# Kernel tuning notes

Measured on AMD Instinct MI355X. Metric: run time of the kernel, lower is better.

Reference implementation:

```python
import jax, jax.numpy as jnp
import numpy as np

N, E, D, A, G, S, NG = 100000, 1600000, 64, 64, 64, 4, 16


def setup_inputs() -> dict:
    key = jax.random.key(0)
    ks = jax.random.split(key, 16)
    x = jax.random.normal(ks[0], (N, D), dtype=jnp.float32)
    x_global = jax.random.normal(ks[1], (NG, G), dtype=jnp.float32)
    edge_attr = jax.random.normal(ks[2], (E, 2), dtype=jnp.float32)
    edge_index = jax.random.randint(ks[3], (2, E), 0, N, dtype=jnp.int32)
    batch_ind = jnp.sort(jax.random.randint(ks[4], (N,), 0, NG, dtype=jnp.int32))
    s = lambda fan: 1.0 / np.sqrt(fan)
    Wm = jax.random.normal(ks[5], (S, D, A), dtype=jnp.float32) * s(D)
    bm = jnp.zeros((S, A), dtype=jnp.float32)
    Wa = jax.random.normal(ks[6], (S, D + G + A, D), dtype=jnp.float32) * s(D + G + A)
    ba = jnp.zeros((S, D), dtype=jnp.float32)
    Wgate = jax.random.normal(ks[7], (S, D, 1), dtype=jnp.float32) * s(D)
    bgate = jnp.zeros((S, 1), dtype=jnp.float32)
    Wfeat = jax.random.normal(ks[8], (S, D, D), dtype=jnp.float32) * s(D)
    bfeat = jnp.zeros((S, D), dtype=jnp.float32)
    Wt = jax.random.normal(ks[9], (S, 2 * G, G), dtype=jnp.float32) * s(2 * G)
    bt = jnp.zeros((S, G), dtype=jnp.float32)
    return {
        'x': x, 'x_global': x_global, 'edge_attr': edge_attr,
        'edge_index': edge_index, 'batch_ind': batch_ind, 'num_graphs': NG,
        'Wm': Wm, 'bm': bm, 'Wa': Wa, 'ba': ba,
        'Wgate': Wgate, 'bgate': bgate, 'Wfeat': Wfeat, 'bfeat': bfeat,
        'Wt': Wt, 'bt': bt,
    }


def reference(x, x_global, edge_attr, edge_index, batch_ind, num_graphs,
              Wm, bm, Wa, ba, Wgate, bgate, Wfeat, bfeat, Wt, bt):
    lrelu = jax.nn.leaky_relu  # negative_slope=0.01, matching torch LeakyReLU
    src, dst = edge_index[0], edge_index[1]
    n_nodes = x.shape[0]
    steps = Wm.shape[0]
    for i in range(steps):
        # --- GraphNet step: gather -> edge MLP -> scatter-max ---
        msg = lrelu(x[src] @ Wm[i] + bm[i])                          # [E, A]
        agg = jax.ops.segment_max(msg, dst, num_segments=n_nodes)    # [N, A]
        agg = jnp.where(jnp.isfinite(agg), agg, 0.0)                 # empty segs -> 0
        xg_b = x_global[batch_ind]                                   # [N, G]
        z = jnp.concatenate([x, xg_b, agg], axis=1)                  # [N, D+G+A]
        x = lrelu(z @ Wa[i] + ba[i]) + x                             # residual
        # --- GlobalNode: attentional (segment-softmax) pooling ---
        gate = x @ Wgate[i] + bgate[i]                               # [N, 1]
        gmax = jax.ops.segment_max(gate, batch_ind, num_segments=num_graphs)
        e = jnp.exp(gate - gmax[batch_ind])
        denom = jax.ops.segment_sum(e, batch_ind, num_segments=num_graphs)
        alpha = e / denom[batch_ind]                                 # [N, 1]
        feat = lrelu(x @ Wfeat[i] + bfeat[i])                        # [N, D]
        xg = jax.ops.segment_sum(alpha * feat, batch_ind, num_segments=num_graphs)
        cat = jnp.concatenate([xg, x_global], axis=1)                # [NG, 2G]
        x_global = lrelu(cat @ Wt[i] + bt[i]) + x_global             # residual
    return x, x_global
```

## Files before the change

kernel.cpp:

```cpp
#include <hip/hip_runtime.h>

#define FD 64
#define NSLOPE 0.01f
#define SCAN_BS 1024

__device__ __forceinline__ float lrelu(float v) { return v > 0.f ? v : NSLOPE * v; }

__device__ __forceinline__ unsigned enc_f32(float f) {
    unsigned u = __float_as_uint(f);
    return (u & 0x80000000u) ? ~u : (u | 0x80000000u);
}
__device__ __forceinline__ float dec_f32(unsigned u) {
    return (u & 0x80000000u) ? __uint_as_float(u & 0x7FFFFFFFu) : __uint_as_float(~u);
}


__global__ void k_hist(const int* __restrict__ dst, int* __restrict__ deg, int E)
{
    int e = blockIdx.x * blockDim.x + threadIdx.x;
    if (e < E) atomicAdd(&deg[dst[e]], 1);
}

__global__ void k_scan1(const int* __restrict__ deg, int* __restrict__ off,
                        int* __restrict__ bsums, int N)
{
    __shared__ int tmp[SCAN_BS];
    int t = threadIdx.x, b = blockIdx.x;
    int i = b * SCAN_BS + t;
    int v = (i < N) ? deg[i] : 0;
    tmp[t] = v;
    __syncthreads();
    for (int d = 1; d < SCAN_BS; d <<= 1) {
        int add = (t >= d) ? tmp[t - d] : 0;
        __syncthreads();
        tmp[t] += add;
        __syncthreads();
    }
    if (i < N) off[i] = tmp[t] - v;
    if (t == SCAN_BS - 1) bsums[b] = tmp[t];
}

__global__ void k_scan2(int* __restrict__ bsums, int nb)
{
    __shared__ int tmp[SCAN_BS];
    int t = threadIdx.x;
    int v = (t < nb) ? bsums[t] : 0;
    tmp[t] = v;
    __syncthreads();
    for (int d = 1; d < SCAN_BS; d <<= 1) {
        int add = (t >= d) ? tmp[t - d] : 0;
        __syncthreads();
        tmp[t] += add;
        __syncthreads();
    }
    if (t < nb) bsums[t] = tmp[t] - v;
}

__global__ void k_scan3(int* __restrict__ off, const int* __restrict__ bsums,
                        int* __restrict__ cursor, int N)
{
    int i = blockIdx.x * blockDim.x + threadIdx.x;
    if (i < N) {
        int o = off[i] + bsums[i >> 10];
        off[i] = o;
        cursor[i] = o;
    }
}

__global__ void k_place(const int* __restrict__ src, const int* __restrict__ dst,
                        int* __restrict__ cursor, int* __restrict__ esrc, int E)
{
    int e = blockIdx.x * blockDim.x + threadIdx.x;
    if (e >= E) return;
    int pos = atomicAdd(&cursor[dst[e]], 1);
    esrc[pos] = src[e];
}


__global__ void k_proj(const float* __restrict__ x, const float* __restrict__ Wm,
                       const float* __restrict__ bm, float* __restrict__ p, int N)
{
    int n = blockIdx.x * blockDim.x + threadIdx.x;
    if (n >= N) return;
    const float* xr = x + (size_t)n * FD;
    float acc[FD];
#pragma unroll
    for (int j = 0; j < FD; ++j) acc[j] = bm[j];
    for (int kt = 0; kt < FD / 8; ++kt) {
        float4 a = *(const float4*)(xr + kt * 8);
        float4 b = *(const float4*)(xr + kt * 8 + 4);
        float z8[8] = {a.x, a.y, a.z, a.w, b.x, b.y, b.z, b.w};
#pragma unroll
        for (int kk = 0; kk < 8; ++kk) {
            const float* wrow = Wm + (kt * 8 + kk) * FD;
#pragma unroll
            for (int j = 0; j < FD; ++j) acc[j] += z8[kk] * wrow[j];
        }
    }
    float* pr = p + (size_t)n * FD;
#pragma unroll
    for (int j = 0; j < FD; ++j) pr[j] = acc[j];
}

__global__ void k_agg(const float4* __restrict__ p4, const int* __restrict__ off,
                      const int* __restrict__ endp, const int* __restrict__ esrc,
                      float4* __restrict__ agg4, int N)
{
    int tid = threadIdx.x;
    int q = tid & 15;
    int n = blockIdx.x * 16 + (tid >> 4);
    if (n >= N) return;
    int j0 = off[n], j1 = endp[n];
    float4 m = make_float4(-__builtin_inff(), -__builtin_inff(),
                           -__builtin_inff(), -__builtin_inff());
    int j = j0;
    for (; j + 1 < j1; j += 2) {
        int s0 = esrc[j], s1 = esrc[j + 1];
        float4 v0 = p4[(size_t)s0 * 16 + q];
        float4 v1 = p4[(size_t)s1 * 16 + q];
        m.x = fmaxf(m.x, v0.x); m.y = fmaxf(m.y, v0.y);
        m.z = fmaxf(m.z, v0.z); m.w = fmaxf(m.w, v0.w);
        m.x = fmaxf(m.x, v1.x); m.y = fmaxf(m.y, v1.y);
        m.z = fmaxf(m.z, v1.z); m.w = fmaxf(m.w, v1.w);
    }
    if (j < j1) {
        int s0 = esrc[j];
        float4 v0 = p4[(size_t)s0 * 16 + q];
        m.x = fmaxf(m.x, v0.x); m.y = fmaxf(m.y, v0.y);
        m.z = fmaxf(m.z, v0.z); m.w = fmaxf(m.w, v0.w);
    }
    float4 o;
    if (j0 == j1) o = make_float4(0.f, 0.f, 0.f, 0.f);
    else { o.x = lrelu(m.x); o.y = lrelu(m.y); o.z = lrelu(m.z); o.w = lrelu(m.w); }
    agg4[(size_t)n * 16 + q] = o;
}

__global__ void k_node(const float* __restrict__ x_in, float* __restrict__ x_out,
                       const float* __restrict__ xg, const int* __restrict__ batch,
                       const float* __restrict__ agg,
                       const float* __restrict__ Wa, const float* __restrict__ ba,
                       const float* __restrict__ Wgate, const float* __restrict__ bgate,
                       const float* __restrict__ Wfeat, const float* __restrict__ bfeat,
                       float* __restrict__ gate_out, float* __restrict__ feat_out,
                       unsigned* __restrict__ gmax_enc, int N)
{
    __shared__ unsigned lmax[16];
    int tid = threadIdx.x;
    if (tid < 16) lmax[tid] = 0u;
    __syncthreads();
    int n = blockIdx.x * blockDim.x + tid;
    if (n < N) {
        int g = batch[n];
        const float* xr  = x_in + (size_t)n * FD;
        const float* xgr = xg + (size_t)g * FD;
        const float* ar  = agg + (size_t)n * FD;
        float acc[FD];
#pragma unroll
        for (int j = 0; j < FD; ++j) acc[j] = ba[j];
        for (int kt = 0; kt < 8; ++kt) {
            float4 a = *(const float4*)(xr + kt * 8);
            float4 b = *(const float4*)(xr + kt * 8 + 4);
            float z8[8] = {a.x, a.y, a.z, a.w, b.x, b.y, b.z, b.w};
#pragma unroll
            for (int kk = 0; kk < 8; ++kk) {
                const float* wrow = Wa + (kt * 8 + kk) * FD;
#pragma unroll
                for (int j = 0; j < FD; ++j) acc[j] += z8[kk] * wrow[j];
            }
        }
        for (int kt = 0; kt < 8; ++kt) {
            float4 a = *(const float4*)(xgr + kt * 8);
            float4 b = *(const float4*)(xgr + kt * 8 + 4);
            float z8[8] = {a.x, a.y, a.z, a.w, b.x, b.y, b.z, b.w};
#pragma unroll
            for (int kk = 0; kk < 8; ++kk) {
                const float* wrow = Wa + (64 + kt * 8 + kk) * FD;
#pragma unroll
                for (int j = 0; j < FD; ++j) acc[j] += z8[kk] * wrow[j];
            }
        }
        for (int kt = 0; kt < 8; ++kt) {
            float4 a = *(const float4*)(ar + kt * 8);
            float4 b = *(const float4*)(ar + kt * 8 + 4);
            float z8[8] = {a.x, a.y, a.z, a.w, b.x, b.y, b.z, b.w};
#pragma unroll
            for (int kk = 0; kk < 8; ++kk) {
                const float* wrow = Wa + (128 + kt * 8 + kk) * FD;
#pragma unroll
                for (int j = 0; j < FD; ++j) acc[j] += z8[kk] * wrow[j];
            }
        }
        float gv = bgate[0];
        float* xo = x_out + (size_t)n * FD;
#pragma unroll
        for (int j = 0; j < FD; ++j) {
            float v = lrelu(acc[j]) + xr[j];
            xo[j] = v;
            gv += v * Wgate[j];
        }
        gate_out[n] = gv;
        atomicMax(&lmax[g], enc_f32(gv));
        float acc2[FD];
#pragma unroll
        for (int j = 0; j < FD; ++j) acc2[j] = bfeat[j];
        for (int kt = 0; kt < 8; ++kt) {
            float4 a = *(const float4*)(xo + kt * 8);
            float4 b = *(const float4*)(xo + kt * 8 + 4);
            float z8[8] = {a.x, a.y, a.z, a.w, b.x, b.y, b.z, b.w};
#pragma unroll
            for (int kk = 0; kk < 8; ++kk) {
                const float* wrow = Wfeat + (kt * 8 + kk) * FD;
#pragma unroll
                for (int j = 0; j < FD; ++j) acc2[j] += z8[kk] * wrow[j];
            }
        }
        float* fo = feat_out + (size_t)n * FD;
#pragma unroll
        for (int j = 0; j < FD; ++j) fo[j] = lrelu(acc2[j]);
    }
    __syncthreads();
    if (tid < 16 && lmax[tid] != 0u) atomicMax(&gmax_enc[tid], lmax[tid]);
}

__global__ void k_pool(const float* __restrict__ gate, const float* __restrict__ feat,
                       const int* __restrict__ batch, const unsigned* __restrict__ gmax_enc,
                       float* __restrict__ sum_e, float* __restrict__ Vv, int N)
{
    int gid = blockIdx.x * blockDim.x + threadIdx.x;
    int wave = gid >> 6;
    int lane = threadIdx.x & 63;
    int nwaves = (gridDim.x * blockDim.x) >> 6;
    int chunk = (N + nwaves - 1) / nwaves;
    int n0 = wave * chunk;
    int n1 = min(N, n0 + chunk);
    if (n0 >= n1) return;
    int gcur = batch[n0];
    float gm = dec_f32(gmax_enc[gcur]);
    float accv = 0.f, acce = 0.f;
    for (int n = n0; n < n1; ++n) {
        int g = batch[n];
        if (g != gcur) {
            atomicAdd(&Vv[gcur * FD + lane], accv);
            if (lane == 0) atomicAdd(&sum_e[gcur], acce);
            gcur = g;
            gm = dec_f32(gmax_enc[g]);
            accv = 0.f; acce = 0.f;
        }
        float e = __expf(gate[n] - gm);
        accv += e * feat[(size_t)n * FD + lane];
        acce += e;
    }
    atomicAdd(&Vv[gcur * FD + lane], accv);
    if (lane == 0) atomicAdd(&sum_e[gcur], acce);
}

__global__ void k_global(const float* __restrict__ xg_in, float* __restrict__ xg_out,
                         const float* __restrict__ Vv, const float* __restrict__ sum_e,
                         const float* __restrict__ Wt, const float* __restrict__ bt, int NG)
{
    __shared__ float xgold[1024], xgn[1024];
    int tid = threadIdx.x;
    int tot = NG * FD;
    if (tid < tot) {
        xgold[tid] = xg_in[tid];
        xgn[tid] = Vv[tid] / sum_e[tid >> 6];
    }
    __syncthreads();
    if (tid >= tot) return;
    int g = tid >> 6, j = tid & 63;
    float acc = bt[j];
    for (int k = 0; k < FD; ++k) acc += xgn[g * FD + k] * Wt[k * FD + j];
    for (int k = 0; k < FD; ++k) acc += xgold[g * FD + k] * Wt[(FD + k) * FD + j];
    xg_out[tid] = lrelu(acc) + xgold[tid];
}

extern "C" void kernel_launch(void* const* d_in, const int* in_sizes, int n_in,
                              void* d_out, int out_size, void* d_ws, size_t ws_size,
                              hipStream_t stream)
{
    const float* x0     = (const float*)d_in[0];
    const float* xg0    = (const float*)d_in[1];
    const int*   ei     = (const int*)d_in[3];
    const int*   batch  = (const int*)d_in[4];
    const float* Wm     = (const float*)d_in[6];
    const float* bm     = (const float*)d_in[7];
    const float* Wa     = (const float*)d_in[8];
    const float* ba     = (const float*)d_in[9];
    const float* Wgate  = (const float*)d_in[10];
    const float* bgate  = (const float*)d_in[11];
    const float* Wfeat  = (const float*)d_in[12];
    const float* bfeat  = (const float*)d_in[13];
    const float* Wt     = (const float*)d_in[14];
    const float* bt     = (const float*)d_in[15];

    const int N  = in_sizes[0] / FD;
    const int E  = in_sizes[3] / 2;
    const int NG = in_sizes[1] / FD;
    const int S  = in_sizes[6] / (FD * FD);

    const int* esrc_in = ei;
    const int* edst_in = ei + E;

    float* x_out  = (float*)d_out;
    float* xg_out = (float*)d_out + (size_t)N * FD;

    char* ws = (char*)d_ws;
    const size_t rowB = (size_t)N * FD * 4;
    float* agg   = (float*)ws;
    float* p     = (float*)(ws + rowB);
    float* feat  = p;
    int*   esrc  = (int*)(ws + 2 * rowB);
    int*   off   = (int*)(ws + 2 * rowB + (size_t)E * 4);
    int*   endp  = off + N;
    int*   deg   = endp + N;
    float* gate  = (float*)deg;
    int*   bsums = deg + N;
    unsigned* gmax_enc = (unsigned*)(bsums + 1024);
    float* sum_e = (float*)(gmax_enc + 64);
    float* Vv    = sum_e + 64;

    const int nb_node = (N + 255) / 256;
    const int nb_edge = (E + 255) / 256;
    const int nb_scan = (N + SCAN_BS - 1) / SCAN_BS;
    const int nb_agg  = (N + 15) / 16;

    hipMemsetAsync(deg, 0, (size_t)N * 4, stream);
    k_hist <<<nb_edge, 256, 0, stream>>>(edst_in, deg, E);
    k_scan1<<<nb_scan, SCAN_BS, 0, stream>>>(deg, off, bsums, N);
    k_scan2<<<1, SCAN_BS, 0, stream>>>(bsums, nb_scan);
    k_scan3<<<nb_node, 256, 0, stream>>>(off, bsums, endp, N);
    k_place<<<nb_edge, 256, 0, stream>>>(esrc_in, edst_in, endp, esrc, E);

    const float* x_in  = x0;
    const float* xg_in = xg0;

    for (int i = 0; i < S; ++i) {
        hipMemsetAsync(gmax_enc, 0, (64 + 64 + 1024) * 4, stream);
        k_proj<<<nb_node, 256, 0, stream>>>(x_in, Wm + i * FD * FD, bm + i * FD, p, N);
        k_agg <<<nb_agg, 256, 0, stream>>>((const float4*)p, off, endp, esrc,
                                           (float4*)agg, N);
        k_node<<<nb_node, 256, 0, stream>>>(x_in, x_out, xg_in, batch, agg,
                                            Wa + (size_t)i * 192 * FD, ba + i * FD,
                                            Wgate + i * FD, bgate + i,
                                            Wfeat + i * FD * FD, bfeat + i * FD,
                                            gate, feat, gmax_enc, N);
        k_pool<<<256, 256, 0, stream>>>(gate, feat, batch, gmax_enc, sum_e, Vv, N);
        k_global<<<1, NG * FD, 0, stream>>>(xg_in, xg_out, Vv, sum_e,
                                            Wt + (size_t)i * 2 * FD * FD, bt + i * FD, NG);
        x_in  = x_out;
        xg_in = xg_out;
    }
}
```

Measured before the change: 1.361 ms.

## Tile node GEMMs through shared memory with 4x4 register blocking

Rewrites k_proj and k_node from one-thread-per-node with a 64-float register accumulator into 64-row block tiles. Activations and weights are staged through shared memory in 16-wide K slices, and each thread keeps a 4x4 output block. The fused node kernel holds the residual output in shared memory so the Wfeat GEMM can reuse it, and computes the gate with a shuffle reduction. This removes heavy register pressure and uncoalesced per-thread row reads, at the cost of extra syncs. k_global is also split into one block per graph.

```diff
diff --git a/kernel.cpp b/kernel.cpp
--- a/kernel.cpp
+++ b/kernel.cpp
@@ -80,26 +80,50 @@
 __global__ void k_proj(const float* __restrict__ x, const float* __restrict__ Wm,
                        const float* __restrict__ bm, float* __restrict__ p, int N)
 {
-    int n = blockIdx.x * blockDim.x + threadIdx.x;
-    if (n >= N) return;
-    const float* xr = x + (size_t)n * FD;
-    float acc[FD];
-#pragma unroll
-    for (int j = 0; j < FD; ++j) acc[j] = bm[j];
-    for (int kt = 0; kt < FD / 8; ++kt) {
-        float4 a = *(const float4*)(xr + kt * 8);
-        float4 b = *(const float4*)(xr + kt * 8 + 4);
-        float z8[8] = {a.x, a.y, a.z, a.w, b.x, b.y, b.z, b.w};
-#pragma unroll
-        for (int kk = 0; kk < 8; ++kk) {
-            const float* wrow = Wm + (kt * 8 + kk) * FD;
-#pragma unroll
-            for (int j = 0; j < FD; ++j) acc[j] += z8[kk] * wrow[j];
-        }
-    }
-    float* pr = p + (size_t)n * FD;
-#pragma unroll
-    for (int j = 0; j < FD; ++j) pr[j] = acc[j];
+    __shared__ float At[16][68];
+    __shared__ float Bt[16][64];
+    const int tid = threadIdx.x;
+    const int tr = tid >> 4, tc = tid & 15;
+    const int n0 = blockIdx.x * 64;
+
+    const int ms = tid >> 2, qs = tid & 3;
+    const int rowc = min(n0 + ms, N - 1);
+    const float* arow = x + (size_t)rowc * FD;
+    const int kks = tid >> 4, js = (tid & 15) * 4;
+
+    float4 bia = *(const float4*)&bm[tc * 4];
+    float acc[4][4];
+#pragma unroll
+    for (int rr = 0; rr < 4; ++rr) { acc[rr][0] = bia.x; acc[rr][1] = bia.y; acc[rr][2] = bia.z; acc[rr][3] = bia.w; }
+
+    for (int ks = 0; ks < 4; ++ks) {
+        int k0 = ks * 16;
+        __syncthreads();
+        float4 av = *(const float4*)(arow + k0 + qs * 4);
+        At[qs * 4 + 0][ms] = av.x; At[qs * 4 + 1][ms] = av.y;
+        At[qs * 4 + 2][ms] = av.z; At[qs * 4 + 3][ms] = av.w;
+        *(float4*)&Bt[kks][js] = *(const float4*)&Wm[(k0 + kks) * FD + js];
+        __syncthreads();
+#pragma unroll
+        for (int k = 0; k < 16; ++k) {
+            float4 a = *(const float4*)&At[k][tr * 4];
+            float4 b = *(const float4*)&Bt[k][tc * 4];
+            float as[4] = {a.x, a.y, a.z, a.w};
+            float bs[4] = {b.x, b.y, b.z, b.w};
+#pragma unroll
+            for (int rr = 0; rr < 4; ++rr)
+#pragma unroll
+                for (int cc = 0; cc < 4; ++cc) acc[rr][cc] += as[rr] * bs[cc];
+        }
+    }
+#pragma unroll
+    for (int rr = 0; rr < 4; ++rr) {
+        int r = tr * 4 + rr;
+        if (n0 + r < N) {
+            float4 o = make_float4(acc[rr][0], acc[rr][1], acc[rr][2], acc[rr][3]);
+            *(float4*)&p[(size_t)(n0 + r) * FD + tc * 4] = o;
+        }
+    }
 }
 
 __global__ void k_agg(const float4* __restrict__ p4, const int* __restrict__ off,
@@ -144,79 +168,114 @@
                        float* __restrict__ gate_out, float* __restrict__ feat_out,
                        unsigned* __restrict__ gmax_enc, int N)
 {
+    __shared__ float At[16][68];
+    __shared__ float Bt[16][64];
+    __shared__ float Xp[64][65];
     __shared__ unsigned lmax[16];
-    int tid = threadIdx.x;
+
+    const int tid = threadIdx.x;
+    const int tr = tid >> 4, tc = tid & 15;
+    const int n0 = blockIdx.x * 64;
     if (tid < 16) lmax[tid] = 0u;
-    __syncthreads();
-    int n = blockIdx.x * blockDim.x + tid;
-    if (n < N) {
-        int g = batch[n];
-        const float* xr  = x_in + (size_t)n * FD;
-        const float* xgr = xg + (size_t)g * FD;
-        const float* ar  = agg + (size_t)n * FD;
-        float acc[FD];
-#pragma unroll
-        for (int j = 0; j < FD; ++j) acc[j] = ba[j];
-        for (int kt = 0; kt < 8; ++kt) {
-            float4 a = *(const float4*)(xr + kt * 8);
-            float4 b = *(const float4*)(xr + kt * 8 + 4);
-            float z8[8] = {a.x, a.y, a.z, a.w, b.x, b.y, b.z, b.w};
-#pragma unroll
-            for (int kk = 0; kk < 8; ++kk) {
-                const float* wrow = Wa + (kt * 8 + kk) * FD;
-#pragma unroll
-                for (int j = 0; j < FD; ++j) acc[j] += z8[kk] * wrow[j];
+
+    const int ms = tid >> 2, qs = tid & 3;
+    const int rowc = min(n0 + ms, N - 1);
+    const float* xrow = x_in + (size_t)rowc * FD;
+    const float* grow = xg + (size_t)batch[rowc] * FD;
+    const float* arow = agg + (size_t)rowc * FD;
+    const int kks = tid >> 4, js = (tid & 15) * 4;
+
+    float4 bia = *(const float4*)&ba[tc * 4];
+    float acc[4][4];
+#pragma unroll
+    for (int rr = 0; rr < 4; ++rr) { acc[rr][0] = bia.x; acc[rr][1] = bia.y; acc[rr][2] = bia.z; acc[rr][3] = bia.w; }
+
+    for (int ks = 0; ks < 12; ++ks) {
+        int k0 = ks * 16;
+        const float* srow = (k0 < 64) ? xrow : (k0 < 128) ? grow : arow;
+        __syncthreads();
+        float4 av = *(const float4*)(srow + (k0 & 63) + qs * 4);
+        At[qs * 4 + 0][ms] = av.x; At[qs * 4 + 1][ms] = av.y;
+        At[qs * 4 + 2][ms] = av.z; At[qs * 4 + 3][ms] = av.w;
+        *(float4*)&Bt[kks][js] = *(const float4*)&Wa[(k0 + kks) * FD + js];
+        __syncthreads();
+#pragma unroll
+        for (int k = 0; k < 16; ++k) {
+            float4 a = *(const float4*)&At[k][tr * 4];
+            float4 b = *(const float4*)&Bt[k][tc * 4];
+            float as[4] = {a.x, a.y, a.z, a.w};
+            float bs[4] = {b.x, b.y, b.z, b.w};
+#pragma unroll
+            for (int rr = 0; rr < 4; ++rr)
+#pragma unroll
+                for (int cc = 0; cc < 4; ++cc) acc[rr][cc] += as[rr] * bs[cc];
+        }
+    }
+
+    float4 wg = *(const float4*)&Wgate[tc * 4];
+    float gpart[4];
+#pragma unroll
+    for (int rr = 0; rr < 4; ++rr) {
+        int r = tr * 4 + rr;
+        float4 xv = *(const float4*)&x_in[(size_t)min(n0 + r, N - 1) * FD + tc * 4];
+        float v0 = lrelu(acc[rr][0]) + xv.x;
+        float v1 = lrelu(acc[rr][1]) + xv.y;
+        float v2 = lrelu(acc[rr][2]) + xv.z;
+        float v3 = lrelu(acc[rr][3]) + xv.w;
+        Xp[r][tc * 4 + 0] = v0; Xp[r][tc * 4 + 1] = v1;
+        Xp[r][tc * 4 + 2] = v2; Xp[r][tc * 4 + 3] = v3;
+        if (n0 + r < N) {
+            float4 o = make_float4(v0, v1, v2, v3);
+            *(float4*)&x_out[(size_t)(n0 + r) * FD + tc * 4] = o;
+        }
+        gpart[rr] = v0 * wg.x + v1 * wg.y + v2 * wg.z + v3 * wg.w;
+    }
+#pragma unroll
+    for (int rr = 0; rr < 4; ++rr) {
+        float g = gpart[rr];
+        g += __shfl_xor(g, 1); g += __shfl_xor(g, 2);
+        g += __shfl_xor(g, 4); g += __shfl_xor(g, 8);
+        if (tc == 0) {
+            int r = tr * 4 + rr;
+            if (n0 + r < N) {
+                float gv = g + bgate[0];
+                gate_out[n0 + r] = gv;
+                atomicMax(&lmax[batch[n0 + r]], enc_f32(gv));
             }
         }
-        for (int kt = 0; kt < 8; ++kt) {
-            float4 a = *(const float4*)(xgr + kt * 8);
-            float4 b = *(const float4*)(xgr + kt * 8 + 4);
-            float z8[8] = {a.x, a.y, a.z, a.w, b.x, b.y, b.z, b.w};
-#pragma unroll
-            for (int kk = 0; kk < 8; ++kk) {
-                const float* wrow = Wa + (64 + kt * 8 + kk) * FD;
-#pragma unroll
-                for (int j = 0; j < FD; ++j) acc[j] += z8[kk] * wrow[j];
-            }
-        }
-        for (int kt = 0; kt < 8; ++kt) {
-            float4 a = *(const float4*)(ar + kt * 8);
-            float4 b = *(const float4*)(ar + kt * 8 + 4);
-            float z8[8] = {a.x, a.y, a.z, a.w, b.x, b.y, b.z, b.w};
-#pragma unroll
-            for (int kk = 0; kk < 8; ++kk) {
-                const float* wrow = Wa + (128 + kt * 8 + kk) * FD;
-#pragma unroll
-                for (int j = 0; j < FD; ++j) acc[j] += z8[kk] * wrow[j];
-            }
-        }
-        float gv = bgate[0];
-        float* xo = x_out + (size_t)n * FD;
-#pragma unroll
-        for (int j = 0; j < FD; ++j) {
-            float v = lrelu(acc[j]) + xr[j];
-            xo[j] = v;
-            gv += v * Wgate[j];
-        }
-        gate_out[n] = gv;
-        atomicMax(&lmax[g], enc_f32(gv));
-        float acc2[FD];
-#pragma unroll
-        for (int j = 0; j < FD; ++j) acc2[j] = bfeat[j];
-        for (int kt = 0; kt < 8; ++kt) {
-            float4 a = *(const float4*)(xo + kt * 8);
-            float4 b = *(const float4*)(xo + kt * 8 + 4);
-            float z8[8] = {a.x, a.y, a.z, a.w, b.x, b.y, b.z, b.w};
-#pragma unroll
-            for (int kk = 0; kk < 8; ++kk) {
-                const float* wrow = Wfeat + (kt * 8 + kk) * FD;
-#pragma unroll
-                for (int j = 0; j < FD; ++j) acc2[j] += z8[kk] * wrow[j];
-            }
-        }
-        float* fo = feat_out + (size_t)n * FD;
-#pragma unroll
-        for (int j = 0; j < FD; ++j) fo[j] = lrelu(acc2[j]);
+    }
+
+    float4 bif = *(const float4*)&bfeat[tc * 4];
+    float acc2[4][4];
+#pragma unroll
+    for (int rr = 0; rr < 4; ++rr) { acc2[rr][0] = bif.x; acc2[rr][1] = bif.y; acc2[rr][2] = bif.z; acc2[rr][3] = bif.w; }
+
+    for (int ks = 0; ks < 4; ++ks) {
+        int k0 = ks * 16;
+        __syncthreads();
+        *(float4*)&Bt[kks][js] = *(const float4*)&Wfeat[(k0 + kks) * FD + js];
+        __syncthreads();
+#pragma unroll
+        for (int k = 0; k < 16; ++k) {
+            float as[4];
+#pragma unroll
+            for (int rr = 0; rr < 4; ++rr) as[rr] = Xp[tr * 4 + rr][k0 + k];
+            float4 b = *(const float4*)&Bt[k][tc * 4];
+            float bs[4] = {b.x, b.y, b.z, b.w};
+#pragma unroll
+            for (int rr = 0; rr < 4; ++rr)
+#pragma unroll
+                for (int cc = 0; cc < 4; ++cc) acc2[rr][cc] += as[rr] * bs[cc];
+        }
+    }
+#pragma unroll
+    for (int rr = 0; rr < 4; ++rr) {
+        int r = tr * 4 + rr;
+        if (n0 + r < N) {
+            float4 o = make_float4(lrelu(acc2[rr][0]), lrelu(acc2[rr][1]),
+                                   lrelu(acc2[rr][2]), lrelu(acc2[rr][3]));
+            *(float4*)&feat_out[(size_t)(n0 + r) * FD + tc * 4] = o;
+        }
     }
     __syncthreads();
     if (tid < 16 && lmax[tid] != 0u) atomicMax(&gmax_enc[tid], lmax[tid]);
@@ -258,20 +317,15 @@
                          const float* __restrict__ Vv, const float* __restrict__ sum_e,
                          const float* __restrict__ Wt, const float* __restrict__ bt, int NG)
 {
-    __shared__ float xgold[1024], xgn[1024];
-    int tid = threadIdx.x;
-    int tot = NG * FD;
-    if (tid < tot) {
-        xgold[tid] = xg_in[tid];
-        xgn[tid] = Vv[tid] / sum_e[tid >> 6];
-    }
+    __shared__ float xgn[FD], xgo[FD];
+    int g = blockIdx.x, j = threadIdx.x;
+    xgn[j] = Vv[g * FD + j] / sum_e[g];
+    xgo[j] = xg_in[g * FD + j];
     __syncthreads();
-    if (tid >= tot) return;
-    int g = tid >> 6, j = tid & 63;
     float acc = bt[j];
-    for (int k = 0; k < FD; ++k) acc += xgn[g * FD + k] * Wt[k * FD + j];
-    for (int k = 0; k < FD; ++k) acc += xgold[g * FD + k] * Wt[(FD + k) * FD + j];
-    xg_out[tid] = lrelu(acc) + xgold[tid];
+    for (int k = 0; k < FD; ++k) acc += xgn[k] * Wt[k * FD + j];
+    for (int k = 0; k < FD; ++k) acc += xgo[k] * Wt[(FD + k) * FD + j];
+    xg_out[g * FD + j] = lrelu(acc) + xgo[j];
 }
 
 extern "C" void kernel_launch(void* const* d_in, const int* in_sizes, int n_in,
@@ -323,6 +377,7 @@
     const int nb_edge = (E + 255) / 256;
     const int nb_scan = (N + SCAN_BS - 1) / SCAN_BS;
     const int nb_agg  = (N + 15) / 16;
+    const int nb_tile = (N + 63) / 64;
 
     hipMemsetAsync(deg, 0, (size_t)N * 4, stream);
     k_hist <<<nb_edge, 256, 0, stream>>>(edst_in, deg, E);
@@ -336,17 +391,17 @@
 
     for (int i = 0; i < S; ++i) {
         hipMemsetAsync(gmax_enc, 0, (64 + 64 + 1024) * 4, stream);
-        k_proj<<<nb_node, 256, 0, stream>>>(x_in, Wm + i * FD * FD, bm + i * FD, p, N);
+        k_proj<<<nb_tile, 256, 0, stream>>>(x_in, Wm + i * FD * FD, bm + i * FD, p, N);
         k_agg <<<nb_agg, 256, 0, stream>>>((const float4*)p, off, endp, esrc,
                                            (float4*)agg, N);
-        k_node<<<nb_node, 256, 0, stream>>>(x_in, x_out, xg_in, batch, agg,
+        k_node<<<nb_tile, 256, 0, stream>>>(x_in, x_out, xg_in, batch, agg,
                                             Wa + (size_t)i * 192 * FD, ba + i * FD,
                                             Wgate + i * FD, bgate + i,
                                             Wfeat + i * FD * FD, bfeat + i * FD,
                                             gate, feat, gmax_enc, N);
         k_pool<<<256, 256, 0, stream>>>(gate, feat, batch, gmax_enc, sum_e, Vv, N);
-        k_global<<<1, NG * FD, 0, stream>>>(xg_in, xg_out, Vv, sum_e,
-                                            Wt + (size_t)i * 2 * FD * FD, bt + i * FD, NG);
+        k_global<<<NG, FD, 0, stream>>>(xg_in, xg_out, Vv, sum_e,
+                                        Wt + (size_t)i * 2 * FD * FD, bt + i * FD, NG);
         x_in  = x_out;
         xg_in = xg_out;
     }
```

Result: slower. 2.985 ms (+119.2%).
